# Kernel optimization log

Measured on AMD Instinct MI355X. Metric: run time of the kernel, lower is better.

## Reference

```python
import jax, jax.numpy as jnp
import numpy as np

TEMP = 0.01            # entropy temperature
THRESH = 0.92          # hamming similarity threshold
BETA = 0.25            # commitment weight
ENT_W = 0.1            # entropy loss weight


def _l2_normalize(x, axis=-1, eps=1e-12):
    n = jnp.sqrt(jnp.sum(x * x, axis=axis, keepdims=True))
    return x / jnp.maximum(n, eps)


def _entropy_loss(affinity):
    # affinity: [N, K] codebook affinities (cosine similarities)
    fa = affinity / TEMP
    probs = jax.nn.softmax(fa, axis=-1)
    log_probs = jax.nn.log_softmax(fa + 1e-5, axis=-1)
    avg_probs = jnp.mean(probs, axis=0)
    avg_entropy = -jnp.sum(avg_probs * jnp.log(avg_probs + 1e-5))
    sample_entropy = -jnp.mean(jnp.sum(probs * log_probs, axis=-1))
    return sample_entropy - avg_entropy


def _hamming_consistency_loss(input_blocks, z_e):
    # binary occupancy: non-air voxels -> 1
    binary = (jnp.argmax(input_blocks, axis=1) != 0).astype(jnp.float32)  # [B,24,24,24]
    B = binary.shape[0]
    # faithful to torch: plain reshapes (no transpose)
    patterns = binary.reshape(B, 6, 4, 6, 4, 6, 4).reshape(B, 6, 6, 6, 64).reshape(-1, 64)
    N = patterns.shape[0]
    P = patterns
    # pairwise hamming distance via two Gram matmuls
    ham = P @ (1.0 - P).T + (1.0 - P) @ P.T          # [N,N]
    sim = 1.0 - ham / 64.0
    mask = (sim > THRESH) & (~jnp.eye(N, dtype=bool))
    W = jax.lax.stop_gradient(jnp.where(mask, sim, 0.0))  # detached weights
    # pre-quant embeddings per chunk, l2-normalized; cosine distance matrix
    emb = jnp.transpose(z_e, (0, 2, 3, 4, 1)).reshape(N, -1)  # [N, C]
    en = _l2_normalize(emb, axis=1)
    cos = en @ en.T                                   # [N,N]
    dist = 1.0 - cos
    return jnp.sum(dist * W) / (jnp.sum(W) + 1e-8)


def setup_inputs() -> dict:
    key = jax.random.key(0)
    k1, k2, k3 = jax.random.split(key, 3)
    input_blocks = jax.random.normal(k1, (16, 32, 24, 24, 24), dtype=jnp.float32)
    z_e = jax.random.normal(k2, (16, 256, 6, 6, 6), dtype=jnp.float32)
    codebook = jax.random.normal(k3, (1024, 256), dtype=jnp.float32)
    return {"input_blocks": input_blocks, "z_e": z_e, "codebook": codebook}


def reference(input_blocks, z_e, codebook):
    B, C, H, W, D = z_e.shape
    z = jnp.transpose(z_e, (0, 2, 3, 4, 1)).reshape(-1, C)   # [N, C]
    zn = _l2_normalize(z, axis=1)
    en = _l2_normalize(codebook, axis=1)                      # [K, C]
    affinity = zn @ en.T                                      # [N, K]
    idx = jnp.argmax(affinity, axis=1)                        # max cosine == min L2 on sphere
    z_q = en[idx]                                             # [N, C]
    sg = jax.lax.stop_gradient
    codebook_loss = jnp.mean((z_q - sg(zn)) ** 2)
    commit_loss = BETA * jnp.mean((sg(z_q) - zn) ** 2)
    ent_loss = ENT_W * _entropy_loss(affinity)
    ham_loss = _hamming_consistency_loss(input_blocks, z_e)
    loss = codebook_loss + commit_loss + ent_loss + ham_loss
    # straight-through estimator
    z_q_ste = zn + sg(z_q - zn)
    z_q_out = jnp.transpose(z_q_ste.reshape(B, H, W, D, C), (0, 4, 1, 2, 3))
    return z_q_out, loss, idx
```

## Files before the change

### kernel.cpp

```cpp
#include <hip/hip_runtime.h>
#include <cstdint>
#include <cstddef>

#define N_ROWS 3456
#define C_DIM 256
#define K_CB 1024
#define B_SZ 16
#define SPATIAL 216
#define VOX 13824
#define NCH 32
#define N_GBLK 108
#define N_FBLK 486

typedef __attribute__((ext_vector_type(16))) float f32x16;
typedef __attribute__((ext_vector_type(8))) short bf16x8;

__device__ __forceinline__ unsigned short f2bf_rne(float f) {
    unsigned int u = __float_as_uint(f);
    u += 0x7FFFu + ((u >> 16) & 1u);
    return (unsigned short)(u >> 16);
}
__device__ __forceinline__ float bf2f(unsigned short h) {
    unsigned int u = ((unsigned int)h) << 16;
    return __uint_as_float(u);
}

__device__ __forceinline__ size_t swz(int n, int c) {
    return (size_t)(n >> 5) * 8192 + (size_t)((c >> 3) * 256) + (size_t)((n & 31) * 8) + (c & 7);
}

__global__ __launch_bounds__(256) void k_pre(
        const float* __restrict__ in, const float* __restrict__ cb,
        const float* __restrict__ ze,
        unsigned long long* __restrict__ pats,
        float* __restrict__ scal,
        float* __restrict__ en,
        unsigned short* __restrict__ ehi, unsigned short* __restrict__ elo,
        unsigned short* __restrict__ zhi, unsigned short* __restrict__ zlo) {
    int bid = blockIdx.x;
    int t = threadIdx.x;
    if (bid < 864) {
        if (bid == 0 && t < 16) scal[t] = 0.0f;
        int v = bid * 256 + t;
        int b = v / VOX;
        int r = v % VOX;
        const float* p = in + (size_t)b * NCH * VOX + r;
        float v0 = p[0];
        float mx = -INFINITY;
#pragma unroll
        for (int c = 1; c < NCH; ++c) mx = fmaxf(mx, p[(size_t)c * VOX]);
        unsigned long long m = __ballot(mx > v0);
        if ((t & 63) == 0) pats[v >> 6] = m;
        return;
    }
    __shared__ float ws[4];
    if (bid < 1888) {
        int k = bid - 864, c = t;
        float v = cb[k * C_DIM + c];
        float ss = v * v;
#pragma unroll
        for (int off = 32; off > 0; off >>= 1) ss += __shfl_down(ss, off, 64);
        if ((c & 63) == 0) ws[c >> 6] = ss;
        __syncthreads();
        float nrm = fmaxf(sqrtf(ws[0] + ws[1] + ws[2] + ws[3]), 1e-12f);
        float o = v / nrm;
        en[k * C_DIM + c] = o;
        unsigned short h = f2bf_rne(o);
        size_t off = swz(k, c);
        ehi[off] = h;
        elo[off] = f2bf_rne(o - bf2f(h));
    } else {
        int n = bid - 1888, c = t;
        int b = n / SPATIAL, s = n % SPATIAL;
        float v = ze[((size_t)(b * C_DIM + c)) * SPATIAL + s];
        float ss = v * v;
#pragma unroll
        for (int off = 32; off > 0; off >>= 1) ss += __shfl_down(ss, off, 64);
        if ((c & 63) == 0) ws[c >> 6] = ss;
        __syncthreads();
        float nrm = fmaxf(sqrtf(ws[0] + ws[1] + ws[2] + ws[3]), 1e-12f);
        float o = v / nrm;
        unsigned short h = f2bf_rne(o);
        size_t off = swz(n, c);
        zhi[off] = h;
        zlo[off] = f2bf_rne(o - bf2f(h));
    }
}

__global__ __launch_bounds__(512, 2) void k_fat(
        const unsigned short* __restrict__ zhi, const unsigned short* __restrict__ zlo,
        const unsigned short* __restrict__ ehi, const unsigned short* __restrict__ elo,
        const unsigned long long* __restrict__ pats,
        const float* __restrict__ en,
        float* __restrict__ avgp_part, float* __restrict__ scal,
        float* __restrict__ out) {
    __shared__ float zq[32 * 257];
    __shared__ float sm[32][8];
    __shared__ int   si[32][8];
    __shared__ float sS[32][8];
    __shared__ float sT[32][8];
    __shared__ float gm[32];
    __shared__ int   gmi[32];
    __shared__ float invS[32];
    __shared__ float ws8[8];
    __shared__ int lastflag;
    unsigned int* done = (unsigned int*)&scal[8];

    int t = threadIdx.x;
    int w = t >> 6, lane = t & 63;
    int half = lane >> 5, l31 = lane & 31;
    int bid = blockIdx.x;
    const bf16x8* __restrict__ Zh = (const bf16x8*)zhi;
    const bf16x8* __restrict__ Zl = (const bf16x8*)zlo;
    const bf16x8* __restrict__ Eh = (const bf16x8*)ehi;
    const bf16x8* __restrict__ El = (const bf16x8*)elo;

    if (bid < N_GBLK) {
        int sa = bid;
        int n0 = bid * 32;

        f32x16 acc[4];
#pragma unroll
        for (int q = 0; q < 4; ++q)
#pragma unroll
            for (int e = 0; e < 16; ++e) acc[q][e] = 0.0f;

#pragma unroll
        for (int s16 = 0; s16 < 16; ++s16) {
            int u = s16 * 64 + lane;
            bf16x8 ah = Zh[(size_t)sa * 1024 + u];
            bf16x8 al = Zl[(size_t)sa * 1024 + u];
            bf16x8 bh[4], bl[4];
#pragma unroll
            for (int q = 0; q < 4; ++q) {
                bh[q] = Eh[(size_t)(w * 4 + q) * 1024 + u];
                bl[q] = El[(size_t)(w * 4 + q) * 1024 + u];
            }
#pragma unroll
            for (int q = 0; q < 4; ++q) {
                acc[q] = __builtin_amdgcn_mfma_f32_32x32x16_bf16(ah, bh[q], acc[q], 0, 0, 0);
                acc[q] = __builtin_amdgcn_mfma_f32_32x32x16_bf16(ah, bl[q], acc[q], 0, 0, 0);
                acc[q] = __builtin_amdgcn_mfma_f32_32x32x16_bf16(al, bh[q], acc[q], 0, 0, 0);
            }
        }

#pragma unroll
        for (int g = 0; g < 16; ++g) {
            float m = acc[0][g];
            int mi = w * 128 + l31;
#pragma unroll
            for (int q = 1; q < 4; ++q) {
                float x = acc[q][g];
                int c = w * 128 + q * 32 + l31;
                if (x > m) { m = x; mi = c; }
            }
#pragma unroll
            for (int mask = 1; mask < 32; mask <<= 1) {
                float vo = __shfl_xor(m, mask, 64);
                int   io = __shfl_xor(mi, mask, 64);
                if (vo > m || (vo == m && io < mi)) { m = vo; mi = io; }
            }
            int row = (g & 3) + 8 * (g >> 2) + 4 * half;
            if (l31 == 0) { sm[row][w] = m; si[row][w] = mi; }
        }
        __syncthreads();

        float cmv = 0.0f;
        if (t < 32) {
            float m = sm[t][0];
            int mi = si[t][0];
#pragma unroll
            for (int ww = 1; ww < 8; ++ww) {
                float mw = sm[t][ww];
                int miw = si[t][ww];
                if (mw > m || (mw == m && miw < mi)) { m = mw; mi = miw; }
            }
            gm[t] = m; gmi[t] = mi;
            out[884737 + n0 + t] = (float)mi;
            cmv = 2.0f - 2.0f * m;
        }
        if (w == 0) {
#pragma unroll
            for (int off = 32; off > 0; off >>= 1) cmv += __shfl_down(cmv, off, 64);
            if (lane == 0) atomicAdd(&scal[1], cmv);
        }
        __syncthreads();

#pragma unroll
        for (int g = 0; g < 16; ++g) {
            int row = (g & 3) + 8 * (g >> 2) + 4 * half;
            float gmr = gm[row];
            float S = 0.0f, T = 0.0f;
#pragma unroll
            for (int q = 0; q < 4; ++q) {
                float d = 100.0f * (acc[q][g] - gmr);
                float ee = __expf(d);
                S += ee; T += ee * d;
                acc[q][g] = ee;
            }
#pragma unroll
            for (int mask = 1; mask < 32; mask <<= 1) {
                S += __shfl_xor(S, mask, 64);
                T += __shfl_xor(T, mask, 64);
            }
            if (l31 == 0) { sS[row][w] = S; sT[row][w] = T; }
        }
#pragma unroll
        for (int rr = 0; rr < 4; ++rr) {
            int row = w * 4 + rr;
            int mi = gmi[row];
            float4 g4 = *(const float4*)&en[(size_t)mi * C_DIM + lane * 4];
            zq[row * 257 + lane * 4 + 0] = g4.x;
            zq[row * 257 + lane * 4 + 1] = g4.y;
            zq[row * 257 + lane * 4 + 2] = g4.z;
            zq[row * 257 + lane * 4 + 3] = g4.w;
        }
        __syncthreads();

        float sev = 0.0f;
        if (t < 32) {
            float S = 0.0f, T = 0.0f;
#pragma unroll
            for (int ww = 0; ww < 8; ++ww) { S += sS[t][ww]; T += sT[t][ww]; }
            float iv = 1.0f / S;
            invS[t] = iv;
            sev = logf(S) - T * iv;
        }
        if (w == 0) {
#pragma unroll
            for (int off = 32; off > 0; off >>= 1) sev += __shfl_down(sev, off, 64);
            if (lane == 0) atomicAdd(&scal[0], sev);
        }
        __syncthreads();

        {
            float cs[4] = {0.0f, 0.0f, 0.0f, 0.0f};
#pragma unroll
            for (int g = 0; g < 16; ++g) {
                int row = (g & 3) + 8 * (g >> 2) + 4 * half;
                float iv = invS[row];
#pragma unroll
                for (int q = 0; q < 4; ++q) cs[q] += acc[q][g] * iv;
            }
#pragma unroll
            for (int q = 0; q < 4; ++q) cs[q] += __shfl_xor(cs[q], 32, 64);
            if (half == 0) {
#pragma unroll
                for (int q = 0; q < 4; ++q)
                    avgp_part[(size_t)bid * K_CB + w * 128 + q * 32 + l31] = cs[q];
            }
        }

        {
            int rl = t & 31, cg = t >> 5;
            int n = n0 + rl;
            int b = n / SPATIAL, s = n - b * SPATIAL;
            size_t obase = ((size_t)b * C_DIM) * SPATIAL + s;
#pragma unroll
            for (int cc = 0; cc < 16; ++cc) {
                int c = cg * 16 + cc;
                out[obase + (size_t)c * SPATIAL] = zq[rl * 257 + c];
            }
        }
    } else if (w < 2) {
        int hb = bid - N_GBLK;
        int ti = 0, rem = hb;
        while (rem >= 27 - ti) { rem -= 27 - ti; ++ti; }
        int tj = ti + rem;
        int i0 = ti * 128, j0 = tj * 128;
        float factor = (ti == tj) ? 1.0f : 2.0f;
        int sib = ti * 4 + w * 2;
        int sjb = tj * 4;

        f32x16 acc[2][4];
#pragma unroll
        for (int a = 0; a < 2; ++a)
#pragma unroll
            for (int b = 0; b < 4; ++b)
#pragma unroll
                for (int e = 0; e < 16; ++e) acc[a][b][e] = 0.0f;

#pragma unroll
        for (int s16 = 0; s16 < 16; ++s16) {
            int u = s16 * 64 + lane;
            bf16x8 a0 = Zh[(size_t)sib * 1024 + u];
            bf16x8 a1 = Zh[(size_t)(sib + 1) * 1024 + u];
            bf16x8 bf[4];
#pragma unroll
            for (int c = 0; c < 4; ++c)
                bf[c] = Zh[(size_t)(sjb + c) * 1024 + u];
#pragma unroll
            for (int c = 0; c < 4; ++c) {
                acc[0][c] = __builtin_amdgcn_mfma_f32_32x32x16_bf16(a0, bf[c], acc[0][c], 0, 0, 0);
                acc[1][c] = __builtin_amdgcn_mfma_f32_32x32x16_bf16(a1, bf[c], acc[1][c], 0, 0, 0);
            }
        }

        unsigned long long pj[4];
#pragma unroll
        for (int c = 0; c < 4; ++c) pj[c] = pats[j0 + c * 32 + l31];

        float sW = 0.0f, sD = 0.0f;
#pragma unroll
        for (int r = 0; r < 2; ++r) {
            int ibase = i0 + w * 64 + r * 32 + 4 * half;
#pragma unroll
            for (int g = 0; g < 16; ++g) {
                int gi = ibase + (g & 3) + 8 * (g >> 2);
                unsigned long long pi = pats[gi];
#pragma unroll
                for (int c = 0; c < 4; ++c) {
                    int gj = j0 + c * 32 + l31;
                    int pop = __popcll(pi ^ pj[c]);
                    float wgt = (pop <= 5 && gi != gj) ? (1.0f - (float)pop * 0.015625f) : 0.0f;
                    sW += wgt;
                    sD += wgt * acc[r][c][g];
                }
            }
        }
#pragma unroll
        for (int off = 32; off > 0; off >>= 1) {
            sW += __shfl_down(sW, off, 64);
            sD += __shfl_down(sD, off, 64);
        }
        if (lane == 0) {
            atomicAdd(&scal[2], factor * sW);
            atomicAdd(&scal[3], factor * sD);
        }
    }

    __syncthreads();
    if (t == 0) {
        __threadfence();
        unsigned int old = atomicAdd(done, 1u);
        lastflag = (old == N_FBLK - 1) ? 1 : 0;
    }
    __syncthreads();
    if (lastflag) {
        __threadfence();
        int col0 = t, col1 = t + 512;
        float p0 = 0.0f, p1 = 0.0f, p2 = 0.0f, p3 = 0.0f;
        float q0 = 0.0f, q1 = 0.0f, q2 = 0.0f, q3 = 0.0f;
        for (int bb = 0; bb < N_GBLK; bb += 4) {
            p0 += avgp_part[(size_t)(bb + 0) * K_CB + col0];
            p1 += avgp_part[(size_t)(bb + 1) * K_CB + col0];
            p2 += avgp_part[(size_t)(bb + 2) * K_CB + col0];
            p3 += avgp_part[(size_t)(bb + 3) * K_CB + col0];
            q0 += avgp_part[(size_t)(bb + 0) * K_CB + col1];
            q1 += avgp_part[(size_t)(bb + 1) * K_CB + col1];
            q2 += avgp_part[(size_t)(bb + 2) * K_CB + col1];
            q3 += avgp_part[(size_t)(bb + 3) * K_CB + col1];
        }
        float ap0 = (p0 + p1 + p2 + p3) * (1.0f / N_ROWS);
        float ap1 = (q0 + q1 + q2 + q3) * (1.0f / N_ROWS);
        float term = ap0 * logf(ap0 + 1e-5f) + ap1 * logf(ap1 + 1e-5f);
#pragma unroll
        for (int off = 32; off > 0; off >>= 1) term += __shfl_down(term, off, 64);
        if (lane == 0) ws8[w] = term;
        __syncthreads();
        if (t == 0) {
            float sAP = 0.0f;
#pragma unroll
            for (int i = 0; i < 8; ++i) sAP += ws8[i];
            float s0 = atomicAdd(&scal[0], 0.0f);
            float s1 = atomicAdd(&scal[1], 0.0f);
            float s2 = atomicAdd(&scal[2], 0.0f);
            float s3 = atomicAdd(&scal[3], 0.0f);
            float sample = s0 * (1.0f / N_ROWS);
            float commit = s1 * (1.0f / ((float)N_ROWS * C_DIM));
            float ent = 0.1f * (sample + sAP);
            float ham = (s2 - s3) / (s2 + 1e-8f);
            out[884736] = 1.25f * commit + ent + ham;
        }
    }
}

extern "C" void kernel_launch(void* const* d_in, const int* in_sizes, int n_in,
                              void* d_out, int out_size, void* d_ws, size_t ws_size,
                              hipStream_t stream) {
    const float* in_blocks = (const float*)d_in[0];
    const float* z_e       = (const float*)d_in[1];
    const float* cb        = (const float*)d_in[2];
    float* out = (float*)d_out;

    char* ws = (char*)d_ws;
    float* en   = (float*)(ws + 0);
    unsigned short* zhi = (unsigned short*)(ws + 15204352);
    unsigned short* zlo = (unsigned short*)(ws + 16973824);
    unsigned short* ehi = (unsigned short*)(ws + 18743296);
    unsigned short* elo = (unsigned short*)(ws + 19267584);
    unsigned long long* pats = (unsigned long long*)(ws + 19791872);
    float* avgp_part = (float*)(ws + 19819520);
    float* scal = (float*)(ws + 20704256);

    k_pre<<<5344, 256, 0, stream>>>(in_blocks, cb, z_e, pats, scal,
                                    en, ehi, elo, zhi, zlo);
    k_fat<<<N_FBLK, 512, 0, stream>>>(zhi, zlo, ehi, elo, pats, en,
                                      avgp_part, scal, out);
}
```

Baseline: 149.5 us.

## Split hamming Gram tiles across all eight waves and batch z normalization

The hamming/cosine tile blocks now use all 8 waves instead of 2. Each wave owns one 32-row strip and half of the K dimension, and the partial sums are combined in shared memory, so each block issues a single pair of atomics. The z_e normalization in the pre-kernel handles 4 spatial rows per block with float4 loads, which cuts that part of the grid by four and makes the reads wider. The launch-bounds occupancy hint of 2 on k_fat is dropped, which lets the compiler use more registers at the risk of lower occupancy.

```diff
diff --git a/kernel.cpp b/kernel.cpp
--- a/kernel.cpp
+++ b/kernel.cpp
@@ -53,7 +53,7 @@
         if ((t & 63) == 0) pats[v >> 6] = m;
         return;
     }
-    __shared__ float ws[4];
+    __shared__ float ws[16];
     if (bid < 1888) {
         int k = bid - 864, c = t;
         float v = cb[k * C_DIM + c];
@@ -70,24 +70,38 @@
         ehi[off] = h;
         elo[off] = f2bf_rne(o - bf2f(h));
     } else {
-        int n = bid - 1888, c = t;
-        int b = n / SPATIAL, s = n % SPATIAL;
-        float v = ze[((size_t)(b * C_DIM + c)) * SPATIAL + s];
-        float ss = v * v;
-#pragma unroll
-        for (int off = 32; off > 0; off >>= 1) ss += __shfl_down(ss, off, 64);
-        if ((c & 63) == 0) ws[c >> 6] = ss;
-        __syncthreads();
-        float nrm = fmaxf(sqrtf(ws[0] + ws[1] + ws[2] + ws[3]), 1e-12f);
-        float o = v / nrm;
-        unsigned short h = f2bf_rne(o);
-        size_t off = swz(n, c);
-        zhi[off] = h;
-        zlo[off] = f2bf_rne(o - bf2f(h));
+        int zb = bid - 1888;
+        int n0 = zb * 4;
+        int b = n0 / SPATIAL, s0 = n0 - b * SPATIAL;
+        int c = t, w = t >> 6, lane = t & 63;
+        float4 v4 = *(const float4*)&ze[((size_t)(b * C_DIM + c)) * SPATIAL + s0];
+        float q0 = v4.x * v4.x, q1 = v4.y * v4.y, q2 = v4.z * v4.z, q3 = v4.w * v4.w;
+#pragma unroll
+        for (int off = 32; off > 0; off >>= 1) {
+            q0 += __shfl_down(q0, off, 64);
+            q1 += __shfl_down(q1, off, 64);
+            q2 += __shfl_down(q2, off, 64);
+            q3 += __shfl_down(q3, off, 64);
+        }
+        if (lane == 0) {
+            ws[w * 4 + 0] = q0; ws[w * 4 + 1] = q1;
+            ws[w * 4 + 2] = q2; ws[w * 4 + 3] = q3;
+        }
+        __syncthreads();
+        float vv[4] = {v4.x, v4.y, v4.z, v4.w};
+#pragma unroll
+        for (int j = 0; j < 4; ++j) {
+            float nrm = fmaxf(sqrtf(ws[j] + ws[4 + j] + ws[8 + j] + ws[12 + j]), 1e-12f);
+            float o = vv[j] / nrm;
+            unsigned short h = f2bf_rne(o);
+            size_t off = swz(n0 + j, c);
+            zhi[off] = h;
+            zlo[off] = f2bf_rne(o - bf2f(h));
+        }
     }
 }
 
-__global__ __launch_bounds__(512, 2) void k_fat(
+__global__ __launch_bounds__(512) void k_fat(
         const unsigned short* __restrict__ zhi, const unsigned short* __restrict__ zlo,
         const unsigned short* __restrict__ ehi, const unsigned short* __restrict__ elo,
         const unsigned long long* __restrict__ pats,
@@ -103,6 +117,7 @@
     __shared__ int   gmi[32];
     __shared__ float invS[32];
     __shared__ float ws8[8];
+    __shared__ float hw8[8], hd8[8];
     __shared__ int lastflag;
     unsigned int* done = (unsigned int*)&scal[8];
 
@@ -262,60 +277,53 @@
                 out[obase + (size_t)c * SPATIAL] = zq[rl * 257 + c];
             }
         }
-    } else if (w < 2) {
+    } else {
         int hb = bid - N_GBLK;
         int ti = 0, rem = hb;
         while (rem >= 27 - ti) { rem -= 27 - ti; ++ti; }
         int tj = ti + rem;
         int i0 = ti * 128, j0 = tj * 128;
         float factor = (ti == tj) ? 1.0f : 2.0f;
-        int sib = ti * 4 + w * 2;
+        int iw = w & 3, kh = w >> 2;
+        int sib = ti * 4 + iw;
         int sjb = tj * 4;
 
-        f32x16 acc[2][4];
-#pragma unroll
-        for (int a = 0; a < 2; ++a)
-#pragma unroll
-            for (int b = 0; b < 4; ++b)
-#pragma unroll
-                for (int e = 0; e < 16; ++e) acc[a][b][e] = 0.0f;
-
-#pragma unroll
-        for (int s16 = 0; s16 < 16; ++s16) {
-            int u = s16 * 64 + lane;
+        f32x16 acc[4];
+#pragma unroll
+        for (int c = 0; c < 4; ++c)
+#pragma unroll
+            for (int e = 0; e < 16; ++e) acc[c][e] = 0.0f;
+
+#pragma unroll
+        for (int s8 = 0; s8 < 8; ++s8) {
+            int u = (kh * 8 + s8) * 64 + lane;
             bf16x8 a0 = Zh[(size_t)sib * 1024 + u];
-            bf16x8 a1 = Zh[(size_t)(sib + 1) * 1024 + u];
             bf16x8 bf[4];
 #pragma unroll
             for (int c = 0; c < 4; ++c)
                 bf[c] = Zh[(size_t)(sjb + c) * 1024 + u];
 #pragma unroll
+            for (int c = 0; c < 4; ++c)
+                acc[c] = __builtin_amdgcn_mfma_f32_32x32x16_bf16(a0, bf[c], acc[c], 0, 0, 0);
+        }
+
+        unsigned long long pj[4];
+#pragma unroll
+        for (int c = 0; c < 4; ++c) pj[c] = pats[j0 + c * 32 + l31];
+
+        float sW = 0.0f, sD = 0.0f;
+        int ibase = i0 + iw * 32 + 4 * half;
+#pragma unroll
+        for (int g = 0; g < 16; ++g) {
+            int gi = ibase + (g & 3) + 8 * (g >> 2);
+            unsigned long long pi = pats[gi];
+#pragma unroll
             for (int c = 0; c < 4; ++c) {
-                acc[0][c] = __builtin_amdgcn_mfma_f32_32x32x16_bf16(a0, bf[c], acc[0][c], 0, 0, 0);
-                acc[1][c] = __builtin_amdgcn_mfma_f32_32x32x16_bf16(a1, bf[c], acc[1][c], 0, 0, 0);
-            }
-        }
-
-        unsigned long long pj[4];
-#pragma unroll
-        for (int c = 0; c < 4; ++c) pj[c] = pats[j0 + c * 32 + l31];
-
-        float sW = 0.0f, sD = 0.0f;
-#pragma unroll
-        for (int r = 0; r < 2; ++r) {
-            int ibase = i0 + w * 64 + r * 32 + 4 * half;
-#pragma unroll
-            for (int g = 0; g < 16; ++g) {
-                int gi = ibase + (g & 3) + 8 * (g >> 2);
-                unsigned long long pi = pats[gi];
-#pragma unroll
-                for (int c = 0; c < 4; ++c) {
-                    int gj = j0 + c * 32 + l31;
-                    int pop = __popcll(pi ^ pj[c]);
-                    float wgt = (pop <= 5 && gi != gj) ? (1.0f - (float)pop * 0.015625f) : 0.0f;
-                    sW += wgt;
-                    sD += wgt * acc[r][c][g];
-                }
+                int gj = j0 + c * 32 + l31;
+                int pop = __popcll(pi ^ pj[c]);
+                float wgt = (pop <= 5 && gi != gj) ? (1.0f - (float)pop * 0.015625f) : 0.0f;
+                sW += wgt;
+                sD += wgt * acc[c][g];
             }
         }
 #pragma unroll
@@ -323,9 +331,14 @@
             sW += __shfl_down(sW, off, 64);
             sD += __shfl_down(sD, off, 64);
         }
-        if (lane == 0) {
-            atomicAdd(&scal[2], factor * sW);
-            atomicAdd(&scal[3], factor * sD);
+        if (lane == 0) { hw8[w] = sW; hd8[w] = sD; }
+        __syncthreads();
+        if (t == 0) {
+            float W = hw8[0] + hw8[1] + hw8[2] + hw8[3];
+            float D = hd8[0] + hd8[1] + hd8[2] + hd8[3]
+                    + hd8[4] + hd8[5] + hd8[6] + hd8[7];
+            atomicAdd(&scal[2], factor * W);
+            atomicAdd(&scal[3], factor * D);
         }
     }
 
@@ -393,7 +406,7 @@
     float* avgp_part = (float*)(ws + 19819520);
     float* scal = (float*)(ws + 20704256);
 
-    k_pre<<<5344, 256, 0, stream>>>(in_blocks, cb, z_e, pats, scal,
+    k_pre<<<2752, 256, 0, stream>>>(in_blocks, cb, z_e, pats, scal,
                                     en, ehi, elo, zhi, zlo);
     k_fat<<<N_FBLK, 512, 0, stream>>>(zhi, zlo, ehi, elo, pats, en,
                                       avgp_part, scal, out);
```

Result: faster. 130.5 us (-12.7%).
